# Optimization experiments

Measured on AMD Instinct MI355X. Metric: run time of the kernel, lower is better.

The kernel has to match this reference:

```python
import jax, jax.numpy as jnp
import numpy as np

BLOCK_SIZE = 4    # MaxPool3d kernel AND patch cube edge (module uses block_size for both)
POOL_STRIDE = 2   # MaxPool3d stride
BLOCK_STRIDE = 2  # patch extraction stride


def setup_inputs() -> dict:
    key = jax.random.key(0)
    x = jax.random.normal(key, (128, 128, 128, 16), dtype=jnp.float32)
    return {"x": x}


def reference(x) -> jnp.ndarray:
    bs, ps, st = BLOCK_SIZE, POOL_STRIDE, BLOCK_STRIDE
    # x: [D,H,W,C] -> [C,D,H,W]
    xc = jnp.transpose(x, (3, 0, 1, 2))
    # MaxPool3d(kernel=block_size, stride=pool_stride), unbatched 4D input
    pooled = jax.lax.reduce_window(
        xc, -jnp.inf, jax.lax.max,
        window_dimensions=(1, bs, bs, bs),
        window_strides=(1, ps, ps, ps),
        padding='VALID')
    # back to [Dp,Hp,Wp,C]
    p = jnp.transpose(pooled, (1, 2, 3, 0))
    Dp, Hp, Wp, C = p.shape
    win = jnp.arange(bs)
    ii = jnp.arange(0, Dp - bs + 1, st)[:, None] + win  # [ni,bs]
    jj = jnp.arange(0, Hp - bs + 1, st)[:, None] + win  # [nj,bs]
    kk = jnp.arange(0, Wp - bs + 1, st)[:, None] + win  # [nk,bs]
    # fused gather replacing the triple python loop
    b = jnp.take(p, ii, axis=0)   # [ni,bs,Hp,Wp,C]
    b = jnp.take(b, jj, axis=2)   # [ni,bs,nj,bs,Wp,C]
    b = jnp.take(b, kk, axis=4)   # [ni,bs,nj,bs,nk,bs,C]
    b = jnp.transpose(b, (0, 2, 4, 1, 3, 5, 6))  # [ni,nj,nk,bs,bs,bs,C]
    n = b.shape[0] * b.shape[1] * b.shape[2]
    # each block flattened row-major over (i,j,k) to (bs^3, C), matching
    # block.contiguous().view(-1, C); blocks stacked in loop order (i,j,k)
    return b.reshape(n, bs * bs * bs, C)
```

## Files before the change

### kernel.cpp

```cpp
#include <hip/hip_runtime.h>
#include <math.h>

#define D0 128
#define NC 16
#define DPE 63
#define NP 30
#define NBLK2 (NP*NP*5)

typedef float f32x4 __attribute__((ext_vector_type(4)));

__device__ __forceinline__ float4 f4max(float4 a, float4 b) {
    return make_float4(fmaxf(a.x, b.x), fmaxf(a.y, b.y), fmaxf(a.z, b.z), fmaxf(a.w, b.w));
}
__device__ __forceinline__ float4 shfl_down4(float4 v, int d) {
    return make_float4(__shfl_down(v.x, d, 64), __shfl_down(v.y, d, 64),
                       __shfl_down(v.z, d, 64), __shfl_down(v.w, d, 64));
}

__global__ __launch_bounds__(576) void hw_pool_stream(const float* __restrict__ x,
                                                      float* __restrict__ hwp) {
    const int bid = blockIdx.x;
    const int d = bid >> 1;
    const int hhalf = bid & 1;
    const int s = threadIdx.x >> 6;
    const int lane = threadIdx.x & 63;
    const int wl = lane >> 2;
    const int c4 = lane & 3;
    const int w = 14 * s + wl;

    const int t0 = hhalf ? 32 : 0;
    const int t1 = hhalf ? 63 : 32;

    const float* base = x + ((size_t)d * D0 * D0 + w) * NC + c4 * 4;
    const size_t rowstep = (size_t)D0 * NC;

    const bool emit = ((wl & 1) == 0) && (wl <= 12);
    const int wp = 7 * s + (wl >> 1);
    float* outb = hwp + ((size_t)d * DPE * DPE + wp) * NC + c4 * 4;

#define LDROW(h) (*reinterpret_cast<const float4*>(base + (size_t)min(h, D0 - 1) * rowstep))
    float4 r0 = LDROW(2 * t0),     r1 = LDROW(2 * t0 + 1);
    float4 n0 = LDROW(2 * t0 + 2), n1 = LDROW(2 * t0 + 3);
    float4 prev = make_float4(-INFINITY, -INFINITY, -INFINITY, -INFINITY);

    for (int t = t0; t <= t1; ++t) {
        float4 nn0 = LDROW(2 * t + 4), nn1 = LDROW(2 * t + 5);
        const float4 pair = f4max(r0, r1);
        if (t > t0) {
            const float4 win = f4max(prev, pair);
            const float4 m1 = f4max(win, shfl_down4(win, 4));
            const float4 m2 = f4max(m1, shfl_down4(m1, 8));
            if (emit)
                *reinterpret_cast<float4*>(outb + (size_t)(t - 1) * (DPE * NC)) = m2;
        }
        prev = pair;
        r0 = n0; r1 = n1; n0 = nn0; n1 = nn1;
    }
#undef LDROW
}

__global__ __launch_bounds__(256) void slab_gather(const float* __restrict__ hwp,
                                                   float* __restrict__ out) {
    const int q = NBLK2 >> 3, r = NBLK2 & 7;
    const int xcd = blockIdx.x & 7, idx = blockIdx.x >> 3;
    const int b = (xcd < r ? xcd * (q + 1) : r * (q + 1) + (xcd - r) * q) + idx;

    const int i = b / 150;
    const int rem = b % 150;
    const int j = rem / 5;
    const int ks = rem % 5;
    const int tid = threadIdx.x;

    __shared__ float4 slab[10 * 4 * 15 * 4];

    for (int it = 0; it < 9; ++it) {
        const int f = tid + 256 * it;
        if (f < 2240) {
            const int d_l = f / 224;
            const int r224 = f - d_l * 224;
            const int hp_l = r224 / 56;
            const int r56 = r224 - hp_l * 56;
            const int wp_l = r56 >> 2;
            const int c4 = f & 3;
            const size_t g = ((size_t)(4 * i + d_l) * DPE + (2 * j + hp_l)) * DPE
                           + (12 * ks + wp_l);
            slab[((d_l * 4 + hp_l) * 15 + wp_l) * 4 + c4] =
                *reinterpret_cast<const float4*>(&hwp[g * NC + c4 * 4]);
        }
    }
    __syncthreads();

    const int a  = (tid >> 6) & 3;
    const int bb = (tid >> 4) & 3;
    const int cc = (tid >> 2) & 3;
    const int c4 = tid & 3;
    const size_t obase = ((size_t)(i * NP + j) * NP + 6 * ks) * 256;
#pragma unroll
    for (int kl = 0; kl < 6; ++kl) {
        const int wp_l = 2 * kl + cc;
        const int base16 = (((2 * a) * 4 + bb) * 15 + wp_l) * 4 + c4;
        float4 m = slab[base16];
        m = f4max(m, slab[base16 + 1 * 240]);
        m = f4max(m, slab[base16 + 2 * 240]);
        m = f4max(m, slab[base16 + 3 * 240]);
        const f32x4 v = {m.x, m.y, m.z, m.w};
        __builtin_nontemporal_store(v, reinterpret_cast<f32x4*>(&out[(obase + kl * 256 + tid) * 4]));
    }
}

__global__ __launch_bounds__(256) void fused_pool_patch(const float* __restrict__ x,
                                                        float* __restrict__ out) {
    const int q = NBLK2 >> 3, r = NBLK2 & 7;
    const int xcd = blockIdx.x & 7, idx = blockIdx.x >> 3;
    const int b = (xcd < r ? xcd * (q + 1) : r * (q + 1) + (xcd - r) * q) + idx;
    const int i  = b / 150;
    const int rem = b % 150;
    const int j  = rem / 5;
    const int ks = rem % 5;
    const int wave = threadIdx.x >> 6;
    const int lane = threadIdx.x & 63;
    const int dg = wave & 1;
    const int wh = wave >> 1;
    const int c4 = lane & 3;
    const int wl = lane >> 2;
    const int w = 24 * ks + 14 * wh + wl;
    const int dbase = 4 * i + 4 * dg;
    const int hbase = 4 * j;
    float4 acc[2][4];
#pragma unroll
    for (int p = 0; p < 2; ++p)
#pragma unroll
        for (int hh = 0; hh < 4; ++hh)
            acc[p][hh] = make_float4(-INFINITY, -INFINITY, -INFINITY, -INFINITY);
#pragma unroll
    for (int dl = 0; dl < 6; ++dl) {
        const size_t rowb = ((size_t)(dbase + dl) * D0 + hbase) * D0 + w;
        float4 rw[10];
#pragma unroll
        for (int hl = 0; hl < 10; ++hl)
            rw[hl] = *reinterpret_cast<const float4*>(&x[(rowb + hl * D0) * NC + c4 * 4]);
#pragma unroll
        for (int hl = 0; hl < 10; ++hl) {
#pragma unroll
            for (int hpl = 0; hpl < 4; ++hpl) {
                if (hl >= 2 * hpl && hl <= 2 * hpl + 3) {
                    if (dl <= 3) acc[0][hpl] = f4max(acc[0][hpl], rw[hl]);
                    if (dl >= 2) acc[1][hpl] = f4max(acc[1][hpl], rw[hl]);
                }
            }
        }
    }
    __shared__ float plds[4 * 4 * 14 * 16];
    const bool emit = ((wl & 1) == 0) && (wl <= 12);
    const int wpl0 = 7 * wh + (wl >> 1);
#pragma unroll
    for (int dpl = 0; dpl < 2; ++dpl) {
#pragma unroll
        for (int hpl = 0; hpl < 4; ++hpl) {
            const float4 v = acc[dpl][hpl];
            const float4 m1 = f4max(v, shfl_down4(v, 4));
            const float4 m2 = f4max(m1, shfl_down4(m1, 8));
            if (emit) {
                const int a = 2 * dg + dpl;
                *reinterpret_cast<float4*>(&plds[(((a * 4 + hpl) * 14 + wpl0) * 4 + c4) * 4]) = m2;
            }
        }
    }
    __syncthreads();
    const size_t obase = ((size_t)(i * 30 + j) * 30 + 6 * ks) * 256;
#pragma unroll
    for (int rr = 0; rr < 6; ++rr) {
        const int f = threadIdx.x + 256 * rr;
        const int rowq = (f >> 2) & 63;
        const int c4e = f & 3;
        const int a  = rowq >> 4;
        const int bbq = (rowq >> 2) & 3;
        const int cc = rowq & 3;
        const int wpl = 2 * (f >> 8) + cc;
        const f32x4 v = *reinterpret_cast<const f32x4*>(
            &plds[(((a * 4 + bbq) * 14 + wpl) * 4 + c4e) * 4]);
        __builtin_nontemporal_store(v, reinterpret_cast<f32x4*>(&out[(obase + f) * 4]));
    }
}

extern "C" void kernel_launch(void* const* d_in, const int* in_sizes, int n_in,
                              void* d_out, int out_size, void* d_ws, size_t ws_size,
                              hipStream_t stream) {
    const float* x = (const float*)d_in[0];
    float* out = (float*)d_out;

    const size_t hwp_bytes = (size_t)D0 * DPE * DPE * NC * sizeof(float);
    if (ws_size >= hwp_bytes) {
        float* hwp = (float*)d_ws;
        hw_pool_stream<<<D0 * 2, 576, 0, stream>>>(x, hwp);
        slab_gather<<<NBLK2, 256, 0, stream>>>(hwp, out);
    } else {
        fused_pool_patch<<<NBLK2, 256, 0, stream>>>(x, out);
    }
}
```

Baseline: 54.97 us.

## Fold depth-pair max into first pass to halve intermediate pooled buffer

The first kernel now reads two adjacent depth slices per block and stores max over both, producing a 63-plane pair-reduced intermediate instead of a 128-plane H/W-pooled buffer. The gather kernel then loads half as much slab data and does a single max over two pair-planes instead of four. This cuts intermediate write and read traffic roughly in half. The first kernel's grid changes to 252 blocks of 16 rows each, and each block now carries twice the loads per iteration.

```diff
diff --git a/kernel.cpp b/kernel.cpp
--- a/kernel.cpp
+++ b/kernel.cpp
@@ -17,50 +17,54 @@
                        __shfl_down(v.z, d, 64), __shfl_down(v.w, d, 64));
 }
 
-__global__ __launch_bounds__(576) void hw_pool_stream(const float* __restrict__ x,
-                                                      float* __restrict__ hwp) {
-    const int bid = blockIdx.x;
-    const int d = bid >> 1;
-    const int hhalf = bid & 1;
+__global__ __launch_bounds__(576) void hw_pool_pair(const float* __restrict__ x,
+                                                    float* __restrict__ hwp2) {
+    const int t = blockIdx.x / 4;
+    const int hq = blockIdx.x & 3;
     const int s = threadIdx.x >> 6;
     const int lane = threadIdx.x & 63;
     const int wl = lane >> 2;
     const int c4 = lane & 3;
     const int w = 14 * s + wl;
 
-    const int t0 = hhalf ? 32 : 0;
-    const int t1 = hhalf ? 63 : 32;
-
-    const float* base = x + ((size_t)d * D0 * D0 + w) * NC + c4 * 4;
+    const int tt0 = 16 * hq;
+    const int tt1 = min(16 * hq + 16, DPE);
+
     const size_t rowstep = (size_t)D0 * NC;
+    const float* base0 = x + ((size_t)(2 * t) * D0 * D0 + w) * NC + c4 * 4;
+    const float* base1 = base0 + (size_t)D0 * D0 * NC;
 
     const bool emit = ((wl & 1) == 0) && (wl <= 12);
     const int wp = 7 * s + (wl >> 1);
-    float* outb = hwp + ((size_t)d * DPE * DPE + wp) * NC + c4 * 4;
-
-#define LDROW(h) (*reinterpret_cast<const float4*>(base + (size_t)min(h, D0 - 1) * rowstep))
-    float4 r0 = LDROW(2 * t0),     r1 = LDROW(2 * t0 + 1);
-    float4 n0 = LDROW(2 * t0 + 2), n1 = LDROW(2 * t0 + 3);
+    float* outb = hwp2 + ((size_t)t * DPE * DPE + wp) * NC + c4 * 4;
+
+#define LDR(B, h) (*reinterpret_cast<const float4*>((B) + (size_t)min(h, D0 - 1) * rowstep))
+    float4 c0 = LDR(base0, 2 * tt0),     c1 = LDR(base0, 2 * tt0 + 1);
+    float4 c2 = LDR(base1, 2 * tt0),     c3 = LDR(base1, 2 * tt0 + 1);
+    float4 n0 = LDR(base0, 2 * tt0 + 2), n1 = LDR(base0, 2 * tt0 + 3);
+    float4 n2 = LDR(base1, 2 * tt0 + 2), n3 = LDR(base1, 2 * tt0 + 3);
     float4 prev = make_float4(-INFINITY, -INFINITY, -INFINITY, -INFINITY);
 
-    for (int t = t0; t <= t1; ++t) {
-        float4 nn0 = LDROW(2 * t + 4), nn1 = LDROW(2 * t + 5);
-        const float4 pair = f4max(r0, r1);
-        if (t > t0) {
+    for (int tt = tt0; tt <= tt1; ++tt) {
+        float4 m0 = LDR(base0, 2 * tt + 4), m1 = LDR(base0, 2 * tt + 5);
+        float4 m2 = LDR(base1, 2 * tt + 4), m3 = LDR(base1, 2 * tt + 5);
+        const float4 pair = f4max(f4max(c0, c1), f4max(c2, c3));
+        if (tt > tt0) {
             const float4 win = f4max(prev, pair);
-            const float4 m1 = f4max(win, shfl_down4(win, 4));
-            const float4 m2 = f4max(m1, shfl_down4(m1, 8));
+            const float4 s1 = f4max(win, shfl_down4(win, 4));
+            const float4 s2 = f4max(s1, shfl_down4(s1, 8));
             if (emit)
-                *reinterpret_cast<float4*>(outb + (size_t)(t - 1) * (DPE * NC)) = m2;
+                *reinterpret_cast<float4*>(outb + (size_t)(tt - 1) * (DPE * NC)) = s2;
         }
         prev = pair;
-        r0 = n0; r1 = n1; n0 = nn0; n1 = nn1;
-    }
-#undef LDROW
-}
-
-__global__ __launch_bounds__(256) void slab_gather(const float* __restrict__ hwp,
-                                                   float* __restrict__ out) {
+        c0 = n0; c1 = n1; c2 = n2; c3 = n3;
+        n0 = m0; n1 = m1; n2 = m2; n3 = m3;
+    }
+#undef LDR
+}
+
+__global__ __launch_bounds__(256) void slab_gather2(const float* __restrict__ hwp2,
+                                                    float* __restrict__ out) {
     const int q = NBLK2 >> 3, r = NBLK2 & 7;
     const int xcd = blockIdx.x & 7, idx = blockIdx.x >> 3;
     const int b = (xcd < r ? xcd * (q + 1) : r * (q + 1) + (xcd - r) * q) + idx;
@@ -71,21 +75,21 @@
     const int ks = rem % 5;
     const int tid = threadIdx.x;
 
-    __shared__ float4 slab[10 * 4 * 15 * 4];
-
-    for (int it = 0; it < 9; ++it) {
+    __shared__ float4 slab[5 * 4 * 15 * 4];
+
+    for (int it = 0; it < 5; ++it) {
         const int f = tid + 256 * it;
-        if (f < 2240) {
-            const int d_l = f / 224;
-            const int r224 = f - d_l * 224;
+        if (f < 1120) {
+            const int t_l = f / 224;
+            const int r224 = f - t_l * 224;
             const int hp_l = r224 / 56;
             const int r56 = r224 - hp_l * 56;
             const int wp_l = r56 >> 2;
             const int c4 = f & 3;
-            const size_t g = ((size_t)(4 * i + d_l) * DPE + (2 * j + hp_l)) * DPE
+            const size_t g = ((size_t)(2 * i + t_l) * DPE + (2 * j + hp_l)) * DPE
                            + (12 * ks + wp_l);
-            slab[((d_l * 4 + hp_l) * 15 + wp_l) * 4 + c4] =
-                *reinterpret_cast<const float4*>(&hwp[g * NC + c4 * 4]);
+            slab[((t_l * 4 + hp_l) * 15 + wp_l) * 4 + c4] =
+                *reinterpret_cast<const float4*>(&hwp2[g * NC + c4 * 4]);
         }
     }
     __syncthreads();
@@ -98,11 +102,8 @@
 #pragma unroll
     for (int kl = 0; kl < 6; ++kl) {
         const int wp_l = 2 * kl + cc;
-        const int base16 = (((2 * a) * 4 + bb) * 15 + wp_l) * 4 + c4;
-        float4 m = slab[base16];
-        m = f4max(m, slab[base16 + 1 * 240]);
-        m = f4max(m, slab[base16 + 2 * 240]);
-        m = f4max(m, slab[base16 + 3 * 240]);
+        const int base16 = ((a * 4 + bb) * 15 + wp_l) * 4 + c4;
+        const float4 m = f4max(slab[base16], slab[base16 + 240]);
         const f32x4 v = {m.x, m.y, m.z, m.w};
         __builtin_nontemporal_store(v, reinterpret_cast<f32x4*>(&out[(obase + kl * 256 + tid) * 4]));
     }
@@ -189,11 +190,11 @@
     const float* x = (const float*)d_in[0];
     float* out = (float*)d_out;
 
-    const size_t hwp_bytes = (size_t)D0 * DPE * DPE * NC * sizeof(float);
-    if (ws_size >= hwp_bytes) {
-        float* hwp = (float*)d_ws;
-        hw_pool_stream<<<D0 * 2, 576, 0, stream>>>(x, hwp);
-        slab_gather<<<NBLK2, 256, 0, stream>>>(hwp, out);
+    const size_t hwp2_bytes = (size_t)DPE * DPE * DPE * NC * sizeof(float);
+    if (ws_size >= hwp2_bytes) {
+        float* hwp2 = (float*)d_ws;
+        hw_pool_pair<<<DPE * 4, 576, 0, stream>>>(x, hwp2);
+        slab_gather2<<<NBLK2, 256, 0, stream>>>(hwp2, out);
     } else {
         fused_pool_patch<<<NBLK2, 256, 0, stream>>>(x, out);
     }
```

After: 50.66 us, median of 2. 7.8% less time.
